# Kernel optimization log

Measured on AMD Instinct MI355X. Metric: run time of the kernel, lower is better.

## Reference

```python
import jax, jax.numpy as jnp
import numpy as np

N = 250000      # total nodes = B * NN
E = 4000000     # edges (avg degree 16)
NODE = 4        # node_size
EDGE = 1        # edge_size
HID = 32        # hidden_dim
NN = 50         # nnodes per graph
NF = 3          # num_factories


def setup_inputs() -> dict:
    key = jax.random.key(0)
    ks = jax.random.split(key, 10)
    def glorot(k, shp, fan_in):
        return (jax.random.normal(k, shp, jnp.float32) / np.sqrt(fan_in)).astype(jnp.float32)
    x = jax.random.normal(ks[0], (N, NODE), jnp.float32)
    edge_index = jax.random.randint(ks[1], (2, E), 0, N, dtype=jnp.int64)
    edge_attr = jax.random.normal(ks[2], (E, EDGE), jnp.float32)
    high = jnp.ones((NF,), jnp.float32)
    D_in = 2 * NODE + EDGE
    D_cat = NODE + HID
    W1 = glorot(ks[3], (D_in, HID), D_in); b1 = jnp.zeros((HID,), jnp.float32)
    W2 = glorot(ks[4], (HID, HID), HID);   b2 = jnp.zeros((HID,), jnp.float32)
    Wc = glorot(ks[5], (D_cat, 1), D_cat);  bc = jnp.zeros((1,), jnp.float32)
    Wmu = glorot(ks[6], (D_cat, 1), D_cat); bmu = jnp.zeros((1,), jnp.float32)
    Wsig = glorot(ks[7], (D_cat, 1), D_cat); bsig = jnp.zeros((1,), jnp.float32)
    return dict(x=x, edge_index=edge_index, edge_attr=edge_attr, high=high,
                W1=W1, b1=b1, W2=W2, b2=b2, Wc=Wc, bc=bc,
                Wmu=Wmu, bmu=bmu, Wsig=Wsig, bsig=bsig)


def reference(x, edge_index, edge_attr, high, W1, b1, W2, b2, Wc, bc, Wmu, bmu, Wsig, bsig):
    # EdgeConv (flow='target_to_source', aggr='add'): x_i = x[row], x_j = x[col], scatter-add at row
    row, col = edge_index[0], edge_index[1]
    msg_in = jnp.concatenate([x[row], x[col], edge_attr], axis=1)      # [E, 2*NODE+EDGE]
    msg = jax.nn.relu(msg_in @ W1 + b1) @ W2 + b2                      # [E, HID]
    agg = jax.ops.segment_sum(msg, row, num_segments=x.shape[0])       # [N, HID]
    x_pp = jnp.concatenate([x, agg], axis=1).reshape(-1, NN, NODE + HID)  # [B, NN, D_cat]
    tail = x_pp[:, -NF:]                                               # [B, NF, D_cat]
    alpha = jax.nn.softplus((tail @ Wmu + bmu).squeeze(-1) + 1e-20) + 1e-20   # [B, NF]
    beta = jax.nn.softplus((tail @ Wsig + bsig).squeeze(-1) + 1e-20) + 1e-20  # [B, NF]
    conc = jax.nn.softplus((x_pp @ Wc + bc).squeeze(-1) + 1e-10)       # [B, NN]
    inventory_act = conc / (conc.sum() + 1e-20)                        # deterministic Dirichlet mean-style
    order_act = alpha / (alpha + beta) * high                          # deterministic Beta mean * high
    return jnp.concatenate([inventory_act, order_act], axis=1)         # [B, NN+NF]
```

## Files before the change

### kernel.cpp

```cpp
#include <hip/hip_runtime.h>

#define N_NODES 250000
#define N_EDGES 4000000
#define HID 32
#define NN 50
#define NF 3
#define OUT_COLS (NN + NF)

#define NB 512
#define NBKT ((N_NODES + NB - 1) / NB)
#define CHUNK 8192
#define NPBLK ((N_EDGES + CHUNK - 1) / CHUNK)
#define BCAP_SLOT 8832
#define RPT_F ((BCAP_SLOT + 511) / 512)

typedef float float2v __attribute__((ext_vector_type(2)));

__device__ __forceinline__ float softplus_f(float v) {
    return fmaxf(v, 0.0f) + log1pf(expf(-fabsf(v)));
}

__device__ __forceinline__ float2v pk_fma(float a, float2v b, float2v c) {
    float2v av = {a, a};
    return __builtin_elementwise_fma(av, b, c);
}

__global__ __launch_bounds__(1024, 8) void part_kernel(
    const int* __restrict__ ei, const float* __restrict__ ea,
    int* __restrict__ gcursor, int2* __restrict__ bpay)
{
    __shared__ int2 srec[CHUNK];
    __shared__ int hist[NBKT];
    __shared__ int excl[NBKT];
    __shared__ int gbase[NBKT];
    __shared__ int asn[NBKT];
    __shared__ unsigned char bkt[CHUNK];
    __shared__ int wsum[16];

    int t = threadIdx.x;
    int lane = t & 63, wid = t >> 6;
    int cbb = blockIdx.x * CHUNK;
    int cnt = N_EDGES - cbb; if (cnt > CHUNK) cnt = CHUNK;

    for (int i = t; i < NBKT; i += 1024) hist[i] = 0;
    __syncthreads();

    int r[CHUNK / 1024];
    #pragma unroll
    for (int j = 0; j < CHUNK / 1024; j++) {
        int o = j * 1024 + t;
        r[j] = (o < cnt) ? ei[cbb + o] : -1;
        if (o < cnt) atomicAdd(&hist[r[j] >> 9], 1);
    }
    __syncthreads();

    int hv = (t < NBKT) ? hist[t] : 0;
    int v = hv;
    #pragma unroll
    for (int off = 1; off < 64; off <<= 1) {
        int u = __shfl_up(v, off, 64);
        if (lane >= off) v += u;
    }
    if (lane == 63) wsum[wid] = v;
    __syncthreads();
    if (wid == 0) {
        int w = (lane < 16) ? wsum[lane] : 0;
        #pragma unroll
        for (int off = 1; off < 16; off <<= 1) {
            int u = __shfl_up(w, off, 64);
            if (lane >= off) w += u;
        }
        if (lane < 16) wsum[lane] = w;
    }
    __syncthreads();
    int wbase = (wid > 0) ? wsum[wid - 1] : 0;
    int myExcl = wbase + (v - hv);
    if (t < NBKT) {
        excl[t] = myExcl;
        asn[t]  = myExcl;
        int base = 0;
        if (hv > 0) base = atomicAdd(&gcursor[t], hv);
        gbase[t] = t * BCAP_SLOT + base;
    }
    __syncthreads();

    #pragma unroll
    for (int j = 0; j < CHUNK / 1024; j++) {
        int o = j * 1024 + t;
        if (o < cnt) {
            int row = r[j];
            int bb = row >> 9;
            int lrow = row & (NB - 1);
            int col  = ei[N_EDGES + cbb + o];
            float at = ea[cbb + o];
            int slot = atomicAdd(&asn[bb], 1);
            srec[slot] = make_int2(col | (lrow << 18), __float_as_int(at));
            bkt[slot] = (unsigned char)(bb & 0xFF);
        }
    }
    __syncthreads();

    for (int s = t; s < cnt; s += 1024) {
        int2 rec = srec[s];
        int c1 = bkt[s];
        int c2 = c1 + 256;
        int bb = (c2 < NBKT && excl[c2] <= s) ? c2 : c1;
        int gpos = gbase[bb] + (s - excl[bb]);
        if (gpos < (bb + 1) * BCAP_SLOT)
            bpay[gpos] = rec;
    }
}

__global__ __launch_bounds__(512, 4) void bucket_kernel(
    const int2* __restrict__ bpay, const int* __restrict__ gcursor,
    const float* __restrict__ x,
    const float* __restrict__ W1, const float* __restrict__ b1,
    const float* __restrict__ W2, const float* __restrict__ b2,
    const float* __restrict__ Wc, const float* __restrict__ bc,
    const float* __restrict__ Wmu, const float* __restrict__ bmu,
    const float* __restrict__ Wsig, const float* __restrict__ bsig,
    const float* __restrict__ high,
    float* __restrict__ sum_out, float* __restrict__ out)
{
    __shared__ int2 srec[BCAP_SLOT];
    __shared__ int hist[NB];
    __shared__ int nbeg[NB];
    __shared__ int cur[NB];
    __shared__ int dhist[64];
    __shared__ int wsum[8];
    __shared__ float bsum[8];

    int b = blockIdx.x;
    int t = threadIdx.x;
    int lane = t & 63, wid = t >> 6;
    int beg = b * BCAP_SLOT;
    int cnt = gcursor[b]; if (cnt > BCAP_SLOT) cnt = BCAP_SLOT;

    hist[t] = 0;
    __syncthreads();

    int2 rec[RPT_F];
    #pragma unroll
    for (int k = 0; k < RPT_F; k++) {
        int s = t + k * 512;
        if (s < cnt) {
            rec[k] = bpay[beg + s];
            atomicAdd(&hist[(rec[k].x >> 18) & (NB - 1)], 1);
        }
    }
    __syncthreads();

    int hv = hist[t];
    int v = hv;
    #pragma unroll
    for (int off = 1; off < 64; off <<= 1) {
        int u = __shfl_up(v, off, 64);
        if (lane >= off) v += u;
    }
    if (lane == 63) wsum[wid] = v;
    __syncthreads();
    if (wid == 0) {
        int w = (lane < 8) ? wsum[lane] : 0;
        #pragma unroll
        for (int off = 1; off < 8; off <<= 1) {
            int u = __shfl_up(w, off, 64);
            if (lane >= off) w += u;
        }
        if (lane < 8) wsum[lane] = w;
    }
    __syncthreads();
    int wbase = (wid > 0) ? wsum[wid - 1] : 0;
    int myExcl = wbase + (v - hv);
    nbeg[t] = myExcl;
    cur[t]  = myExcl;
    __syncthreads();

    #pragma unroll
    for (int k = 0; k < RPT_F; k++) {
        int s = t + k * 512;
        if (s < cnt) {
            int lrow = (rec[k].x >> 18) & (NB - 1);
            int pos = atomicAdd(&cur[lrow], 1);
            srec[pos] = rec[k];
        }
    }

    int bin = min(hv, 63);
    if (t < 64) dhist[t] = 0;
    __syncthreads();
    atomicAdd(&dhist[bin], 1);
    __syncthreads();
    if (wid == 0) {
        int dv = dhist[lane];
        int sv = dv;
        #pragma unroll
        for (int off = 1; off < 64; off <<= 1) {
            int u = __shfl_up(sv, off, 64);
            if (lane >= off) sv += u;
        }
        dhist[lane] = sv - dv;
    }
    __syncthreads();
    int pos = atomicAdd(&dhist[bin], 1);
    cur[pos] = t;
    __syncthreads();

    int tt = cur[t];
    int n = b * NB + tt;
    bool valid = (n < N_NODES);
    int nn = valid ? n : 0;
    int deg = valid ? hist[tt] : 0;
    int s0 = nbeg[tt];

    float4 xr = *(const float4*)(x + 4 * (size_t)nn);

    const float2v* W1v = (const float2v*)W1;
    const float2v* b1v = (const float2v*)b1;

    float2v arow[16];
    #pragma unroll
    for (int k2 = 0; k2 < 16; k2++) {
        float2v a = b1v[k2];
        a = pk_fma(xr.x, W1v[0 * 16 + k2], a);
        a = pk_fma(xr.y, W1v[1 * 16 + k2], a);
        a = pk_fma(xr.z, W1v[2 * 16 + k2], a);
        a = pk_fma(xr.w, W1v[3 * 16 + k2], a);
        arow[k2] = a;
    }

    float2v acc2[16];
    #pragma unroll
    for (int j2 = 0; j2 < 16; j2++) { float2v z = {0.f, 0.f}; acc2[j2] = z; }

    float mk0[4], ev0[4];
    float4 xc0[4];
    #pragma unroll
    for (int j = 0; j < 4; j++) {
        bool ok = j < deg;
        int idx = ok ? (s0 + j) : 0;
        int2 rr = srec[idx];
        mk0[j] = ok ? 1.0f : 0.0f;
        int col = ok ? (rr.x & 0x3FFFF) : 0;
        ev0[j] = ok ? __int_as_float(rr.y) : 0.0f;
        xc0[j] = *(const float4*)(x + 4 * (size_t)col);
    }

    for (int c = 0; c < deg; c += 4) {
        int c1 = c + 4;
        float mk1[4], ev1[4];
        float4 xc1[4];
        #pragma unroll
        for (int j = 0; j < 4; j++) {
            bool ok = (c1 + j) < deg;
            int idx = ok ? (s0 + c1 + j) : 0;
            int2 rr = srec[idx];
            mk1[j] = ok ? 1.0f : 0.0f;
            int col = ok ? (rr.x & 0x3FFFF) : 0;
            ev1[j] = ok ? __int_as_float(rr.y) : 0.0f;
            xc1[j] = *(const float4*)(x + 4 * (size_t)col);
        }

        #pragma unroll
        for (int k2 = 0; k2 < 16; k2++) {
            float2v w4 = W1v[4 * 16 + k2];
            float2v w5 = W1v[5 * 16 + k2];
            float2v w6 = W1v[6 * 16 + k2];
            float2v w7 = W1v[7 * 16 + k2];
            float2v w8 = W1v[8 * 16 + k2];
            #pragma unroll
            for (int j = 0; j < 4; j++) {
                float2v a = arow[k2];
                a = pk_fma(xc0[j].x, w4, a);
                a = pk_fma(xc0[j].y, w5, a);
                a = pk_fma(xc0[j].z, w6, a);
                a = pk_fma(xc0[j].w, w7, a);
                a = pk_fma(ev0[j],   w8, a);
                float2v zero = {0.0f, 0.0f};
                a = __builtin_elementwise_max(a, zero);
                float2v mm = {mk0[j], mk0[j]};
                acc2[k2] = __builtin_elementwise_fma(a, mm, acc2[k2]);
            }
        }

        #pragma unroll
        for (int j = 0; j < 4; j++) {
            mk0[j] = mk1[j]; ev0[j] = ev1[j]; xc0[j] = xc1[j];
        }
    }

    float c_val = 0.0f;
    if (valid) {
        float* accf = (float*)acc2;
        float fdeg = (float)deg;
        float aout[32];
        #pragma unroll
        for (int j = 0; j < 32; j++) aout[j] = fdeg * b2[j];
        for (int k = 0; k < 32; k++) {
            float sk = accf[k];
            #pragma unroll
            for (int j = 0; j < 32; j++) aout[j] = fmaf(sk, W2[k * 32 + j], aout[j]);
        }

        float zc = bc[0];
        zc = fmaf(xr.x, Wc[0], zc);
        zc = fmaf(xr.y, Wc[1], zc);
        zc = fmaf(xr.z, Wc[2], zc);
        zc = fmaf(xr.w, Wc[3], zc);
        #pragma unroll
        for (int j = 0; j < 32; j++) zc = fmaf(aout[j], Wc[4 + j], zc);
        c_val = softplus_f(zc + 1e-10f);

        int g = n / NN;
        int i = n - g * NN;
        out[(size_t)g * OUT_COLS + i] = c_val;

        if (i >= NN - NF) {
            float zm = bmu[0], zs = bsig[0];
            zm = fmaf(xr.x, Wmu[0], zm);   zs = fmaf(xr.x, Wsig[0], zs);
            zm = fmaf(xr.y, Wmu[1], zm);   zs = fmaf(xr.y, Wsig[1], zs);
            zm = fmaf(xr.z, Wmu[2], zm);   zs = fmaf(xr.z, Wsig[2], zs);
            zm = fmaf(xr.w, Wmu[3], zm);   zs = fmaf(xr.w, Wsig[3], zs);
            #pragma unroll
            for (int j = 0; j < 32; j++) {
                zm = fmaf(aout[j], Wmu[4 + j], zm);
                zs = fmaf(aout[j], Wsig[4 + j], zs);
            }
            float alpha = softplus_f(zm + 1e-20f) + 1e-20f;
            float beta  = softplus_f(zs + 1e-20f) + 1e-20f;
            int k = i - (NN - NF);
            out[(size_t)g * OUT_COLS + NN + k] = alpha / (alpha + beta) * high[k];
        }
    }

    float s = c_val;
    #pragma unroll
    for (int off = 32; off > 0; off >>= 1) s += __shfl_down(s, off, 64);
    if (lane == 0) bsum[wid] = s;
    __syncthreads();
    if (t == 0) {
        float tt2 = 0.0f;
        #pragma unroll
        for (int j = 0; j < 8; j++) tt2 += bsum[j];
        atomicAdd(sum_out, tt2);
    }
}

__global__ __launch_bounds__(256) void div_kernel(
    const float* __restrict__ sum_in, float* __restrict__ out)
{
    int n = blockIdx.x * 256 + threadIdx.x;
    if (n >= N_NODES) return;
    float inv = 1.0f / (*sum_in + 1e-20f);
    int g = n / NN;
    int i = n - g * NN;
    out[(size_t)g * OUT_COLS + i] *= inv;
}

extern "C" void kernel_launch(void* const* d_in, const int* in_sizes, int n_in,
                              void* d_out, int out_size, void* d_ws, size_t ws_size,
                              hipStream_t stream)
{
    const float* x    = (const float*)d_in[0];
    const int*   ei   = (const int*)d_in[1];
    const float* ea   = (const float*)d_in[2];
    const float* high = (const float*)d_in[3];
    const float* W1   = (const float*)d_in[4];
    const float* b1   = (const float*)d_in[5];
    const float* W2   = (const float*)d_in[6];
    const float* b2   = (const float*)d_in[7];
    const float* Wc   = (const float*)d_in[8];
    const float* bc   = (const float*)d_in[9];
    const float* Wmu  = (const float*)d_in[10];
    const float* bmu  = (const float*)d_in[11];
    const float* Wsig = (const float*)d_in[12];
    const float* bsig = (const float*)d_in[13];
    float* out = (float*)d_out;

    char* ws = (char*)d_ws;
    int2*  bpay    = (int2*)ws;
    int*   gcursor = (int*)(ws + 34550784);
    float* ssum    = (float*)(ws + 34552832);

    hipMemsetAsync(gcursor, 0, 2048, stream);
    hipMemsetAsync(ssum, 0, 4, stream);

    part_kernel<<<NPBLK, 1024, 0, stream>>>(ei, ea, gcursor, bpay);
    bucket_kernel<<<NBKT, 512, 0, stream>>>(
        bpay, gcursor, x, W1, b1, W2, b2, Wc, bc, Wmu, bmu, Wsig, bsig,
        high, ssum, out);
    div_kernel<<<(N_NODES + 255) / 256, 256, 0, stream>>>(ssum, out);
}
```

Measured before the change: 191.5 us.

## Fuse normalization into bucket kernel via grid barrier and reuse atomic ranks

Each thread keeps the rank returned by the histogram atomicAdd in both kernels and uses it to place records directly, which removes the second pass of shared-memory atomics. The separate division kernel is removed: every bucket block adds its partial sum, then waits on a global done counter with a spin barrier and scales its own outputs by the inverse total. The two memsets are also merged into one. The spin barrier assumes all 489 blocks are co-resident, which 512-thread blocks with about 70KB of LDS may not guarantee, so it risks deadlock or idle waiting while blocks spin.

```diff
diff --git a/kernel.cpp b/kernel.cpp
--- a/kernel.cpp
+++ b/kernel.cpp
@@ -33,7 +33,6 @@
     __shared__ int hist[NBKT];
     __shared__ int excl[NBKT];
     __shared__ int gbase[NBKT];
-    __shared__ int asn[NBKT];
     __shared__ unsigned char bkt[CHUNK];
     __shared__ int wsum[16];
 
@@ -46,11 +45,12 @@
     __syncthreads();
 
     int r[CHUNK / 1024];
+    int rk[CHUNK / 1024];
     #pragma unroll
     for (int j = 0; j < CHUNK / 1024; j++) {
         int o = j * 1024 + t;
         r[j] = (o < cnt) ? ei[cbb + o] : -1;
-        if (o < cnt) atomicAdd(&hist[r[j] >> 9], 1);
+        rk[j] = (o < cnt) ? atomicAdd(&hist[r[j] >> 9], 1) : 0;
     }
     __syncthreads();
 
@@ -77,7 +77,6 @@
     int myExcl = wbase + (v - hv);
     if (t < NBKT) {
         excl[t] = myExcl;
-        asn[t]  = myExcl;
         int base = 0;
         if (hv > 0) base = atomicAdd(&gcursor[t], hv);
         gbase[t] = t * BCAP_SLOT + base;
@@ -93,7 +92,7 @@
             int lrow = row & (NB - 1);
             int col  = ei[N_EDGES + cbb + o];
             float at = ea[cbb + o];
-            int slot = atomicAdd(&asn[bb], 1);
+            int slot = excl[bb] + rk[j];
             srec[slot] = make_int2(col | (lrow << 18), __float_as_int(at));
             bkt[slot] = (unsigned char)(bb & 0xFF);
         }
@@ -120,15 +119,17 @@
     const float* __restrict__ Wmu, const float* __restrict__ bmu,
     const float* __restrict__ Wsig, const float* __restrict__ bsig,
     const float* __restrict__ high,
-    float* __restrict__ sum_out, float* __restrict__ out)
+    float* __restrict__ sum_out, int* __restrict__ done_flag,
+    float* __restrict__ out)
 {
     __shared__ int2 srec[BCAP_SLOT];
     __shared__ int hist[NB];
     __shared__ int nbeg[NB];
-    __shared__ int cur[NB];
+    __shared__ int perm[NB];
     __shared__ int dhist[64];
     __shared__ int wsum[8];
     __shared__ float bsum[8];
+    __shared__ float s_inv;
 
     int b = blockIdx.x;
     int t = threadIdx.x;
@@ -140,12 +141,13 @@
     __syncthreads();
 
     int2 rec[RPT_F];
+    int rk[RPT_F];
     #pragma unroll
     for (int k = 0; k < RPT_F; k++) {
         int s = t + k * 512;
         if (s < cnt) {
             rec[k] = bpay[beg + s];
-            atomicAdd(&hist[(rec[k].x >> 18) & (NB - 1)], 1);
+            rk[k] = atomicAdd(&hist[(rec[k].x >> 18) & (NB - 1)], 1);
         }
     }
     __syncthreads();
@@ -170,9 +172,7 @@
     }
     __syncthreads();
     int wbase = (wid > 0) ? wsum[wid - 1] : 0;
-    int myExcl = wbase + (v - hv);
-    nbeg[t] = myExcl;
-    cur[t]  = myExcl;
+    nbeg[t] = wbase + (v - hv);
     __syncthreads();
 
     #pragma unroll
@@ -180,8 +180,7 @@
         int s = t + k * 512;
         if (s < cnt) {
             int lrow = (rec[k].x >> 18) & (NB - 1);
-            int pos = atomicAdd(&cur[lrow], 1);
-            srec[pos] = rec[k];
+            srec[nbeg[lrow] + rk[k]] = rec[k];
         }
     }
 
@@ -202,10 +201,10 @@
     }
     __syncthreads();
     int pos = atomicAdd(&dhist[bin], 1);
-    cur[pos] = t;
-    __syncthreads();
-
-    int tt = cur[t];
+    perm[pos] = t;
+    __syncthreads();
+
+    int tt = perm[t];
     int n = b * NB + tt;
     bool valid = (n < N_NODES);
     int nn = valid ? n : 0;
@@ -289,6 +288,7 @@
     }
 
     float c_val = 0.0f;
+    int g = 0, i = 0;
     if (valid) {
         float* accf = (float*)acc2;
         float fdeg = (float)deg;
@@ -310,9 +310,8 @@
         for (int j = 0; j < 32; j++) zc = fmaf(aout[j], Wc[4 + j], zc);
         c_val = softplus_f(zc + 1e-10f);
 
-        int g = n / NN;
-        int i = n - g * NN;
-        out[(size_t)g * OUT_COLS + i] = c_val;
+        g = n / NN;
+        i = n - g * NN;
 
         if (i >= NN - NF) {
             float zm = bmu[0], zs = bsig[0];
@@ -337,23 +336,25 @@
     for (int off = 32; off > 0; off >>= 1) s += __shfl_down(s, off, 64);
     if (lane == 0) bsum[wid] = s;
     __syncthreads();
+
     if (t == 0) {
         float tt2 = 0.0f;
         #pragma unroll
         for (int j = 0; j < 8; j++) tt2 += bsum[j];
         atomicAdd(sum_out, tt2);
-    }
-}
-
-__global__ __launch_bounds__(256) void div_kernel(
-    const float* __restrict__ sum_in, float* __restrict__ out)
-{
-    int n = blockIdx.x * 256 + threadIdx.x;
-    if (n >= N_NODES) return;
-    float inv = 1.0f / (*sum_in + 1e-20f);
-    int g = n / NN;
-    int i = n - g * NN;
-    out[(size_t)g * OUT_COLS + i] *= inv;
+        __threadfence();
+        atomicAdd(done_flag, 1);
+        while (__hip_atomic_load(done_flag, __ATOMIC_ACQUIRE,
+                                 __HIP_MEMORY_SCOPE_AGENT) < NBKT)
+            __builtin_amdgcn_s_sleep(2);
+        float sv = __hip_atomic_load(sum_out, __ATOMIC_RELAXED,
+                                     __HIP_MEMORY_SCOPE_AGENT);
+        s_inv = 1.0f / (sv + 1e-20f);
+    }
+    __syncthreads();
+
+    if (valid)
+        out[(size_t)g * OUT_COLS + i] = c_val * s_inv;
 }
 
 extern "C" void kernel_launch(void* const* d_in, const int* in_sizes, int n_in,
@@ -380,13 +381,12 @@
     int2*  bpay    = (int2*)ws;
     int*   gcursor = (int*)(ws + 34550784);
     float* ssum    = (float*)(ws + 34552832);
-
-    hipMemsetAsync(gcursor, 0, 2048, stream);
-    hipMemsetAsync(ssum, 0, 4, stream);
+    int*   done    = (int*)(ws + 34552836);
+
+    hipMemsetAsync(gcursor, 0, 2056, stream);
 
     part_kernel<<<NPBLK, 1024, 0, stream>>>(ei, ea, gcursor, bpay);
     bucket_kernel<<<NBKT, 512, 0, stream>>>(
         bpay, gcursor, x, W1, b1, W2, b2, Wc, bc, Wmu, bmu, Wsig, bsig,
-        high, ssum, out);
-    div_kernel<<<(N_NODES + 255) / 256, 256, 0, stream>>>(ssum, out);
-}
+        high, ssum, done, out);
+}
```

Result: slower. 284.2 us (+48.4%).

## Fold W2 into output heads and reuse histogram ranks instead of second atomics

Applied to the files above, without the earlier changes.

Precomputes W2·Wc, W2·Wmu, W2·Wsig and b2·W products per block in shared memory, so each node no longer runs the 32x32 W2 matmul and only needs 32-wide dot products. Both kernels keep the rank returned by the histogram atomicAdd and use it to compute scatter slots directly, removing the second round of shared atomics. The two memsets are merged into one, relying on ssum sitting right after gcursor in the workspace. The risks are slightly different floating-point summation order and a little extra per-block setup work.

```diff
diff --git a/kernel.cpp b/kernel.cpp
--- a/kernel.cpp
+++ b/kernel.cpp
@@ -33,7 +33,6 @@
     __shared__ int hist[NBKT];
     __shared__ int excl[NBKT];
     __shared__ int gbase[NBKT];
-    __shared__ int asn[NBKT];
     __shared__ unsigned char bkt[CHUNK];
     __shared__ int wsum[16];
 
@@ -46,11 +45,12 @@
     __syncthreads();
 
     int r[CHUNK / 1024];
+    int rk[CHUNK / 1024];
     #pragma unroll
     for (int j = 0; j < CHUNK / 1024; j++) {
         int o = j * 1024 + t;
         r[j] = (o < cnt) ? ei[cbb + o] : -1;
-        if (o < cnt) atomicAdd(&hist[r[j] >> 9], 1);
+        rk[j] = (o < cnt) ? atomicAdd(&hist[r[j] >> 9], 1) : 0;
     }
     __syncthreads();
 
@@ -77,7 +77,6 @@
     int myExcl = wbase + (v - hv);
     if (t < NBKT) {
         excl[t] = myExcl;
-        asn[t]  = myExcl;
         int base = 0;
         if (hv > 0) base = atomicAdd(&gcursor[t], hv);
         gbase[t] = t * BCAP_SLOT + base;
@@ -93,7 +92,7 @@
             int lrow = row & (NB - 1);
             int col  = ei[N_EDGES + cbb + o];
             float at = ea[cbb + o];
-            int slot = atomicAdd(&asn[bb], 1);
+            int slot = excl[bb] + rk[j];
             srec[slot] = make_int2(col | (lrow << 18), __float_as_int(at));
             bkt[slot] = (unsigned char)(bb & 0xFF);
         }
@@ -125,10 +124,12 @@
     __shared__ int2 srec[BCAP_SLOT];
     __shared__ int hist[NB];
     __shared__ int nbeg[NB];
-    __shared__ int cur[NB];
+    __shared__ int perm[NB];
     __shared__ int dhist[64];
     __shared__ int wsum[8];
     __shared__ float bsum[8];
+    __shared__ float fW[3][32];
+    __shared__ float fB[3];
 
     int b = blockIdx.x;
     int t = threadIdx.x;
@@ -137,15 +138,32 @@
     int cnt = gcursor[b]; if (cnt > BCAP_SLOT) cnt = BCAP_SLOT;
 
     hist[t] = 0;
+    if (t < 96) {
+        int vsel = t >> 5;
+        int k = t & 31;
+        const float* Wv = (vsel == 0) ? Wc : (vsel == 1) ? Wmu : Wsig;
+        float f = 0.0f;
+        #pragma unroll
+        for (int j = 0; j < 32; j++) f = fmaf(W2[k * 32 + j], Wv[4 + j], f);
+        fW[vsel][k] = f;
+    } else if (t < 99) {
+        int vsel = t - 96;
+        const float* Wv = (vsel == 0) ? Wc : (vsel == 1) ? Wmu : Wsig;
+        float f = 0.0f;
+        #pragma unroll
+        for (int j = 0; j < 32; j++) f = fmaf(b2[j], Wv[4 + j], f);
+        fB[vsel] = f;
+    }
     __syncthreads();
 
     int2 rec[RPT_F];
+    int rk[RPT_F];
     #pragma unroll
     for (int k = 0; k < RPT_F; k++) {
         int s = t + k * 512;
         if (s < cnt) {
             rec[k] = bpay[beg + s];
-            atomicAdd(&hist[(rec[k].x >> 18) & (NB - 1)], 1);
+            rk[k] = atomicAdd(&hist[(rec[k].x >> 18) & (NB - 1)], 1);
         }
     }
     __syncthreads();
@@ -170,9 +188,7 @@
     }
     __syncthreads();
     int wbase = (wid > 0) ? wsum[wid - 1] : 0;
-    int myExcl = wbase + (v - hv);
-    nbeg[t] = myExcl;
-    cur[t]  = myExcl;
+    nbeg[t] = wbase + (v - hv);
     __syncthreads();
 
     #pragma unroll
@@ -180,8 +196,7 @@
         int s = t + k * 512;
         if (s < cnt) {
             int lrow = (rec[k].x >> 18) & (NB - 1);
-            int pos = atomicAdd(&cur[lrow], 1);
-            srec[pos] = rec[k];
+            srec[nbeg[lrow] + rk[k]] = rec[k];
         }
     }
 
@@ -202,10 +217,10 @@
     }
     __syncthreads();
     int pos = atomicAdd(&dhist[bin], 1);
-    cur[pos] = t;
-    __syncthreads();
-
-    int tt = cur[t];
+    perm[pos] = t;
+    __syncthreads();
+
+    int tt = perm[t];
     int n = b * NB + tt;
     bool valid = (n < N_NODES);
     int nn = valid ? n : 0;
@@ -292,22 +307,14 @@
     if (valid) {
         float* accf = (float*)acc2;
         float fdeg = (float)deg;
-        float aout[32];
-        #pragma unroll
-        for (int j = 0; j < 32; j++) aout[j] = fdeg * b2[j];
-        for (int k = 0; k < 32; k++) {
-            float sk = accf[k];
-            #pragma unroll
-            for (int j = 0; j < 32; j++) aout[j] = fmaf(sk, W2[k * 32 + j], aout[j]);
-        }
-
-        float zc = bc[0];
+
+        float zc = fmaf(fdeg, fB[0], bc[0]);
         zc = fmaf(xr.x, Wc[0], zc);
         zc = fmaf(xr.y, Wc[1], zc);
         zc = fmaf(xr.z, Wc[2], zc);
         zc = fmaf(xr.w, Wc[3], zc);
         #pragma unroll
-        for (int j = 0; j < 32; j++) zc = fmaf(aout[j], Wc[4 + j], zc);
+        for (int j = 0; j < 32; j++) zc = fmaf(accf[j], fW[0][j], zc);
         c_val = softplus_f(zc + 1e-10f);
 
         int g = n / NN;
@@ -315,15 +322,16 @@
         out[(size_t)g * OUT_COLS + i] = c_val;
 
         if (i >= NN - NF) {
-            float zm = bmu[0], zs = bsig[0];
+            float zm = fmaf(fdeg, fB[1], bmu[0]);
+            float zs = fmaf(fdeg, fB[2], bsig[0]);
             zm = fmaf(xr.x, Wmu[0], zm);   zs = fmaf(xr.x, Wsig[0], zs);
             zm = fmaf(xr.y, Wmu[1], zm);   zs = fmaf(xr.y, Wsig[1], zs);
             zm = fmaf(xr.z, Wmu[2], zm);   zs = fmaf(xr.z, Wsig[2], zs);
             zm = fmaf(xr.w, Wmu[3], zm);   zs = fmaf(xr.w, Wsig[3], zs);
             #pragma unroll
             for (int j = 0; j < 32; j++) {
-                zm = fmaf(aout[j], Wmu[4 + j], zm);
-                zs = fmaf(aout[j], Wsig[4 + j], zs);
+                zm = fmaf(accf[j], fW[1][j], zm);
+                zs = fmaf(accf[j], fW[2][j], zs);
             }
             float alpha = softplus_f(zm + 1e-20f) + 1e-20f;
             float beta  = softplus_f(zs + 1e-20f) + 1e-20f;
@@ -381,8 +389,7 @@
     int*   gcursor = (int*)(ws + 34550784);
     float* ssum    = (float*)(ws + 34552832);
 
-    hipMemsetAsync(gcursor, 0, 2048, stream);
-    hipMemsetAsync(ssum, 0, 4, stream);
+    hipMemsetAsync(gcursor, 0, 2052, stream);
 
     part_kernel<<<NPBLK, 1024, 0, stream>>>(ei, ea, gcursor, bpay);
     bucket_kernel<<<NBKT, 512, 0, stream>>>(
```

Result: no change. 189.0 us (-1.3%).
